# Kernel optimization log

Measured on AMD Instinct MI355X. Metric: run time of the kernel, lower is better.

## Reference

```python
import jax, jax.numpy as jnp
import numpy as np

B, C, H, W = 4, 256, 64, 64
CC = 32      # cond_channels
RATE = 2     # cond_downscale_rate
G = 8        # deformable_groups
K = 9        # 3x3 kernel positions
GN = 32      # GroupNorm groups
EPS = 1e-6


def conv2d(x, w, b, pad, groups=1):
    y = jax.lax.conv_general_dilated(x, w, (1, 1), [(pad, pad), (pad, pad)],
                                     feature_group_count=groups,
                                     dimension_numbers=('NCHW', 'OIHW', 'NCHW'))
    return y + b[None, :, None, None]


def group_norm(x, gamma, beta):
    b, c, h, w = x.shape
    xr = x.reshape(b, GN, c // GN, h, w)
    mu = xr.mean(axis=(2, 3, 4), keepdims=True)
    var = xr.var(axis=(2, 3, 4), keepdims=True)
    xn = ((xr - mu) * jax.lax.rsqrt(var + EPS)).reshape(b, c, h, w)
    return xn * gamma[None, :, None, None] + beta[None, :, None, None]


def bilinear_gather(img, y, x):
    # img [B,G,Cg,H,W]; y,x [B,G,Ho,Wo] -> [B,G,Cg,Ho,Wo], zeros outside
    Bb, Gg, Cg, Hh, Ww = img.shape
    Ho, Wo = y.shape[2], y.shape[3]
    y0 = jnp.floor(y); x0 = jnp.floor(x)
    wy1 = y - y0; wx1 = x - x0
    flat = img.reshape(Bb, Gg, Cg, Hh * Ww)

    def g(yi, xi):
        valid = (yi >= 0) & (yi <= Hh - 1) & (xi >= 0) & (xi <= Ww - 1)
        yc = jnp.clip(yi, 0, Hh - 1).astype(jnp.int32)
        xc = jnp.clip(xi, 0, Ww - 1).astype(jnp.int32)
        idx = (yc * Ww + xc).reshape(Bb, Gg, 1, Ho * Wo)
        v = jnp.take_along_axis(flat, jnp.broadcast_to(idx, (Bb, Gg, Cg, Ho * Wo)), axis=3)
        return v.reshape(Bb, Gg, Cg, Ho, Wo) * valid[:, :, None].astype(img.dtype)

    w00 = ((1 - wy1) * (1 - wx1))[:, :, None]
    w01 = ((1 - wy1) * wx1)[:, :, None]
    w10 = (wy1 * (1 - wx1))[:, :, None]
    w11 = (wy1 * wx1)[:, :, None]
    return w00 * g(y0, x0) + w01 * g(y0, x0 + 1) + w10 * g(y0 + 1, x0) + w11 * g(y0 + 1, x0 + 1)


def resize_bilinear(x, rate):
    # F.interpolate(..., mode='bilinear', align_corners=False), integer downscale
    b, c, h, w = x.shape
    ho, wo = h // rate, w // rate
    ys = (jnp.arange(ho, dtype=x.dtype) + 0.5) * rate - 0.5
    xs = (jnp.arange(wo, dtype=x.dtype) + 0.5) * rate - 0.5
    yy = jnp.broadcast_to(ys[:, None], (ho, wo))[None, None]
    xx = jnp.broadcast_to(xs[None, :], (ho, wo))[None, None]
    yy = jnp.broadcast_to(yy, (b, 1, ho, wo))
    xx = jnp.broadcast_to(xx, (b, 1, ho, wo))
    return bilinear_gather(x[:, None], yy, xx)[:, 0]


def deform_conv2d(x, offset, mask, w, b):
    # modulated deformable conv, 3x3, stride 1, pad 1 (torchvision semantics)
    Bb, Cin, Hh, Ww = x.shape
    Cg = Cin // G
    Cout = w.shape[0]
    xr = x.reshape(Bb, G, Cg, Hh, Ww)
    off = offset.reshape(Bb, G, K, 2, Hh, Ww)   # [..., (dy,dx), H, W]
    m = jax.nn.sigmoid(mask).reshape(Bb, G, K, Hh, Ww)
    base_y = jnp.arange(Hh, dtype=x.dtype)[:, None]
    base_x = jnp.arange(Ww, dtype=x.dtype)[None, :]
    acc = jnp.zeros((Bb, Cout, Hh, Ww), x.dtype)
    for k in range(K):
        kh, kw = k // 3 - 1, k % 3 - 1
        yy = base_y + kh + off[:, :, k, 0]
        xx = base_x + kw + off[:, :, k, 1]
        s = bilinear_gather(xr, yy, xx) * m[:, :, k][:, :, None]
        wk = w[:, :, kh + 1, kw + 1].reshape(Cout, G, Cg)
        acc = acc + jnp.einsum('bgchw,ogc->bohw', s, wk)
    return acc + b[None, :, None, None]


def setup_inputs() -> dict:
    key = jax.random.key(0)
    ks = jax.random.split(key, 8)
    d = {}
    d['x_main'] = jax.random.normal(ks[0], (B, C, H, W), jnp.float32)
    d['inpfeat'] = jax.random.normal(ks[1], (B, CC, H * RATE, W * RATE), jnp.float32)
    d['w1a'] = jax.random.normal(ks[2], (C, C + CC, 1, 1), jnp.float32) * (1.0 / np.sqrt(C + CC))
    d['b1a'] = jnp.zeros((C,), jnp.float32)
    d['g1'] = jnp.ones((C,), jnp.float32); d['be1'] = jnp.zeros((C,), jnp.float32)
    d['w1b'] = jax.random.normal(ks[3], (C, 1, 7, 7), jnp.float32) * (1.0 / 7.0)
    d['b1b'] = jnp.zeros((C,), jnp.float32)
    d['g2'] = jnp.ones((C,), jnp.float32); d['be2'] = jnp.zeros((C,), jnp.float32)
    d['w1c'] = jax.random.normal(ks[4], (C, C, 1, 1), jnp.float32) * (1.0 / np.sqrt(C))
    d['b1c'] = jnp.zeros((C,), jnp.float32)
    d['w2'] = jax.random.normal(ks[5], (C, C, 3, 3), jnp.float32) * (1.0 / np.sqrt(9 * C))
    d['b2'] = jnp.zeros((C,), jnp.float32)
    d['g3'] = jnp.ones((C,), jnp.float32); d['be3'] = jnp.zeros((C,), jnp.float32)
    d['w_off'] = jax.random.normal(ks[6], (3 * G * K, C, 3, 3), jnp.float32) * 0.01
    d['b_off'] = jnp.zeros((3 * G * K,), jnp.float32)
    d['w_dcn'] = jax.random.normal(ks[7], (C, C, 3, 3), jnp.float32) * (1.0 / np.sqrt(9 * C))
    d['b_dcn'] = jnp.zeros((C,), jnp.float32)
    return d


def reference(x_main, inpfeat, w1a, b1a, g1, be1, w1b, b1b, g2, be2, w1c, b1c,
              w2, b2, g3, be3, w_off, b_off, w_dcn, b_dcn):
    inp = resize_bilinear(inpfeat, RATE)                       # [B,CC,H,W]
    f = conv2d(jnp.concatenate([inp, x_main], axis=1), w1a, b1a, 0)
    f = jax.nn.silu(group_norm(f, g1, be1))
    f = conv2d(f, w1b, b1b, 3, groups=C)                       # depthwise 7x7
    f = jax.nn.silu(group_norm(f, g2, be2))
    f = conv2d(f, w1c, b1c, 0)
    off_feat = jax.nn.silu(group_norm(conv2d(f, w2, b2, 1), g3, be3))
    co = conv2d(off_feat, w_off, b_off, 1)                     # [B, 3*G*K, H, W]
    o1, o2, mk = jnp.split(co, 3, axis=1)
    offset = jnp.concatenate([o1, o2], axis=1)
    warp_feat = deform_conv2d(x_main, offset, mk, w_dcn, b_dcn)
    return warp_feat, off_feat
```

## Files before the change

kernel.cpp:

```cpp
#include <hip/hip_runtime.h>
#include <math.h>

constexpr int B = 4, C = 256, CC = 32, H = 64, W = 64, HW = H * W;
constexpr int G = 8, K = 9, GN = 32, CPG = C / GN;
constexpr int OFFC = 3 * G * K;

typedef __attribute__((ext_vector_type(8))) short short8;
typedef __attribute__((ext_vector_type(4))) float f32x4;

__device__ inline short f2bf(float f) {
  unsigned u = __builtin_bit_cast(unsigned, f);
  return (short)((u + 0x7FFFu + ((u >> 16) & 1u)) >> 16);
}
__device__ inline float bf2f(short s) {
  unsigned u = ((unsigned)(unsigned short)s) << 16;
  return __builtin_bit_cast(float, u);
}

__global__ void k_prep(const float* __restrict__ w1a, short* __restrict__ wT1a,
                       const float* __restrict__ w1c, short* __restrict__ wT1c,
                       const float* __restrict__ w2, short* __restrict__ wT2,
                       const float* __restrict__ woff, short* __restrict__ wToff,
                       const float* __restrict__ wdcn, short* __restrict__ wTd,
                       float* __restrict__ sbuf) {
  int id = blockIdx.x * 256 + threadIdx.x;
  if (id < 73728) {
    wT1a[id] = f2bf(w1a[id]);
  } else if (id < 139264) {
    int i = id - 73728;
    wT1c[i] = f2bf(w1c[i]);
  } else if (id < 204800) {
    int i = id - 139264;
    int o = i >> 8, ci = i & 255;
    #pragma unroll
    for (int k = 0; k < 9; ++k)
      wT2[((size_t)k * 256 + o) * 256 + ci] = f2bf(w2[(size_t)i * 9 + k]);
  } else if (id < 260096) {
    int i = id - 204800;
    int o = i / 256, ci = i % 256;
    #pragma unroll
    for (int k = 0; k < 9; ++k)
      wToff[((size_t)k * 216 + o) * 256 + ci] = f2bf(woff[(size_t)i * 9 + k]);
  } else if (id < 325632) {
    int i = id - 260096;
    int o = i >> 8, ci = i & 255;
    int g = ci >> 5, cg = ci & 31;
    #pragma unroll
    for (int k = 0; k < 9; ++k)
      wTd[(((size_t)g * 9 + k) * 256 + o) * 32 + cg] = f2bf(wdcn[(size_t)i * 9 + k]);
  } else if (id < 326400) {
    sbuf[id - 325632] = 0.f;
  }
}

__global__ void k_resizeT(const float* __restrict__ in, short* __restrict__ dst) {
  int t = threadIdx.x;
  int p0 = blockIdx.x * 64;
  int b = blockIdx.y;
  int px = t >> 2, cq = t & 3;
  int p = p0 + px;
  int y = p >> 6, x = p & 63;
  short8 v;
  #pragma unroll
  for (int j = 0; j < 8; ++j) {
    int c = cq * 8 + j;
    const float* src = in + ((size_t)b * CC + c) * (2 * H) * (2 * W) + (2 * y) * (2 * W) + 2 * x;
    v[j] = f2bf(0.25f * (src[0] + src[1] + src[2 * W] + src[2 * W + 1]));
  }
  *(short8*)(dst + ((size_t)b * HW + p) * 288 + cq * 8) = v;
}

__global__ void k_transpose(const float* __restrict__ src, short* __restrict__ dst,
                            int Csrc, int Cdst, int coff) {
  int t = threadIdx.x;
  int p0 = blockIdx.x * 64;
  int cc0 = blockIdx.y * 32;
  int b = blockIdx.z;
  int px = t >> 2, cq = t & 3;
  const float* s = src + ((size_t)b * Csrc + cc0 + cq * 8) * HW + p0 + px;
  short8 v;
  #pragma unroll
  for (int j = 0; j < 8; ++j) v[j] = f2bf(s[(size_t)j * HW]);
  *(short8*)(dst + ((size_t)b * HW + p0 + px) * Cdst + coff + cc0 + cq * 8) = v;
}

template<int CIN, int OUT_BF16>
__global__ __launch_bounds__(256) void k_conv1x1_mfma(
    const short* __restrict__ gT, const short* __restrict__ wT,
    const float* __restrict__ bias, void* __restrict__ outp) {
  const int tid = threadIdx.x;
  const int lane = tid & 63, wv = tid >> 6;
  const int l15 = lane & 15, l4 = lane >> 4;
  const int lin = blockIdx.x + gridDim.x * (blockIdx.y + gridDim.y * blockIdx.z);
  const int nb = gridDim.x * gridDim.y * gridDim.z;
  const int swz = (lin & 7) * (nb >> 3) + (lin >> 3);
  const int bx = swz % gridDim.x;
  const int rem = swz / gridDim.x;
  const int b = rem / gridDim.y;
  const int o0 = (rem % gridDim.y) * 64;
  const int p0 = bx * 128;

  const short* gTb = gT + (size_t)b * HW * CIN;
  const short* br[2];
  #pragma unroll
  for (int nt = 0; nt < 2; ++nt)
    br[nt] = gTb + (size_t)(p0 + wv * 32 + nt * 16 + l15) * CIN;
  const short* ar[4];
  #pragma unroll
  for (int mt = 0; mt < 4; ++mt)
    ar[mt] = wT + (size_t)(o0 + mt * 16 + l15) * CIN;

  f32x4 acc[4][2];
  #pragma unroll
  for (int mt = 0; mt < 4; ++mt)
    #pragma unroll
    for (int nt = 0; nt < 2; ++nt) acc[mt][nt] = (f32x4)0.f;

  short8 a_c[4], b_c[2], a_n[4], b_n[2];
  #pragma unroll
  for (int mt = 0; mt < 4; ++mt) a_c[mt] = *(const short8*)(ar[mt] + l4 * 8);
  #pragma unroll
  for (int nt = 0; nt < 2; ++nt) b_c[nt] = *(const short8*)(br[nt] + l4 * 8);

  for (int ck = 0; ck < CIN / 32; ++ck) {
    if (ck + 1 < CIN / 32) {
      int cin_n = (ck + 1) * 32 + l4 * 8;
      #pragma unroll
      for (int mt = 0; mt < 4; ++mt) a_n[mt] = *(const short8*)(ar[mt] + cin_n);
      #pragma unroll
      for (int nt = 0; nt < 2; ++nt) b_n[nt] = *(const short8*)(br[nt] + cin_n);
    }
    #pragma unroll
    for (int mt = 0; mt < 4; ++mt)
      #pragma unroll
      for (int nt = 0; nt < 2; ++nt)
        acc[mt][nt] = __builtin_amdgcn_mfma_f32_16x16x32_bf16(
            a_c[mt], b_c[nt], acc[mt][nt], 0, 0, 0);
    if (ck + 1 < CIN / 32) {
      #pragma unroll
      for (int mt = 0; mt < 4; ++mt) a_c[mt] = a_n[mt];
      #pragma unroll
      for (int nt = 0; nt < 2; ++nt) b_c[nt] = b_n[nt];
    }
  }

  #pragma unroll
  for (int mt = 0; mt < 4; ++mt) {
    #pragma unroll
    for (int nt = 0; nt < 2; ++nt) {
      int p = p0 + wv * 32 + nt * 16 + l15;
      if (OUT_BF16) {
        short4 vv;
        #pragma unroll
        for (int r = 0; r < 4; ++r) {
          int oo = o0 + mt * 16 + l4 * 4 + r;
          ((short*)&vv)[r] = f2bf(acc[mt][nt][r] + bias[oo]);
        }
        *(short4*)((short*)outp + ((size_t)b * HW + p) * 256 + o0 + mt * 16 + l4 * 4) = vv;
      } else {
        float* out = (float*)outp;
        #pragma unroll
        for (int r = 0; r < 4; ++r) {
          int oo = o0 + mt * 16 + l4 * 4 + r;
          out[((size_t)b * 256 + oo) * HW + p] = acc[mt][nt][r] + bias[oo];
        }
      }
    }
  }
}

template<int CIN, int COUT>
__global__ __launch_bounds__(512, 4) void k_mfma_conv9(
    const short* __restrict__ gT, const short* __restrict__ wT,
    const float* __restrict__ bias, float* __restrict__ out) {
  constexpr int POS = 4 * 66;
  constexpr int PSTR = 40;
  __shared__ short lds[2][POS * PSTR];
  const int tid = threadIdx.x;
  const int lane = tid & 63, wv = tid >> 6;
  const int l15 = lane & 15, l4 = lane >> 4;
  const int lin = blockIdx.x + gridDim.x * (blockIdx.y + gridDim.y * blockIdx.z);
  const int nb = gridDim.x * gridDim.y * gridDim.z;
  const int swz = (lin & 7) * (nb >> 3) + (lin >> 3);
  const int bx = swz % gridDim.x;
  const int rem = swz / gridDim.x;
  const int b = rem / gridDim.y;
  const int o0 = (rem % gridDim.y) * 64;
  const int p0 = bx * 128;
  const int y0 = p0 >> 6;
  const bool producer = (wv >= 4);
  const int pid = tid - 256;
  const int cwv = wv;

  const short* gTb = gT + (size_t)b * HW * CIN;

  auto stage = [&](int ck, short* sb) {
    const int ci0 = ck * 32;
    #pragma unroll
    for (int j = 0; j < 5; ++j) {
      int i = pid + j * 256;
      if (i < POS * 4) {
        int pos = i >> 2, cq = i & 3;
        short8 v = {0, 0, 0, 0, 0, 0, 0, 0};
        int r = pos / 66;
        int cx = pos - r * 66 - 1;
        int y = y0 - 1 + r;
        if ((unsigned)y < (unsigned)H && (unsigned)cx < (unsigned)W)
          v = *(const short8*)(gTb + (size_t)(y * W + cx) * CIN + ci0 + cq * 8);
        *(short8*)(sb + pos * PSTR + cq * 8) = v;
      }
    }
  };

  f32x4 acc[4][2];
  #pragma unroll
  for (int mt = 0; mt < 4; ++mt)
    #pragma unroll
    for (int nt = 0; nt < 2; ++nt) acc[mt][nt] = (f32x4)0.f;

  if (producer) stage(0, lds[0]);
  __syncthreads();
  for (int ck = 0; ck < CIN / 32; ++ck) {
    if (producer) {
      if (ck + 1 < CIN / 32) stage(ck + 1, lds[(ck + 1) & 1]);
    } else {
      const int ci0 = ck * 32;
      const short* sb = lds[ck & 1];
      for (int tap = 0; tap < 9; ++tap) {
        short8 a[4];
        #pragma unroll
        for (int mt = 0; mt < 4; ++mt) {
          int o_r = o0 + mt * 16 + l15;
          if (COUT % 64 == 0 || o_r < COUT)
            a[mt] = *(const short8*)(wT + ((size_t)tap * COUT + o_r) * CIN + ci0 + l4 * 8);
          else
            a[mt] = (short8){0, 0, 0, 0, 0, 0, 0, 0};
        }
        short8 bb[2];
        #pragma unroll
        for (int nt = 0; nt < 2; ++nt) {
          int dy = tap / 3 - 1, dx = tap % 3 - 1;
          int row = (cwv >> 1) + dy + 1;
          int col = (cwv & 1) * 32 + nt * 16 + l15 + dx + 1;
          bb[nt] = *(const short8*)(sb + (row * 66 + col) * PSTR + l4 * 8);
        }
        #pragma unroll
        for (int mt = 0; mt < 4; ++mt)
          #pragma unroll
          for (int nt = 0; nt < 2; ++nt)
            acc[mt][nt] = __builtin_amdgcn_mfma_f32_16x16x32_bf16(
                a[mt], bb[nt], acc[mt][nt], 0, 0, 0);
      }
    }
    __syncthreads();
  }

  if (!producer) {
    #pragma unroll
    for (int mt = 0; mt < 4; ++mt) {
      #pragma unroll
      for (int nt = 0; nt < 2; ++nt) {
        int p = p0 + cwv * 32 + nt * 16 + l15;
        #pragma unroll
        for (int r = 0; r < 4; ++r) {
          int oo = o0 + mt * 16 + l4 * 4 + r;
          if (COUT % 64 == 0 || oo < COUT)
            out[((size_t)b * COUT + oo) * HW + p] = acc[mt][nt][r] + bias[oo];
        }
      }
    }
  }
}

__global__ void k_gn_stats_part(const float* __restrict__ in,
                                float* __restrict__ ssum, float* __restrict__ ssq) {
  int g = blockIdx.x, b = blockIdx.y, z = blockIdx.z;
  const float4* base = (const float4*)(in + ((size_t)b * C + g * CPG) * HW) + z * 2048;
  float s = 0.f, s2 = 0.f;
  for (int i = threadIdx.x; i < 2048; i += 256) {
    float4 v = base[i];
    s  += v.x + v.y + v.z + v.w;
    s2 += v.x * v.x + v.y * v.y + v.z * v.z + v.w * v.w;
  }
  #pragma unroll
  for (int off = 32; off > 0; off >>= 1) {
    s  += __shfl_down(s, off);
    s2 += __shfl_down(s2, off);
  }
  __shared__ float sh[8];
  int wid = threadIdx.x >> 6, lane = threadIdx.x & 63;
  if (lane == 0) { sh[wid] = s; sh[4 + wid] = s2; }
  __syncthreads();
  if (threadIdx.x == 0) {
    atomicAdd(&ssum[b * GN + g], sh[0] + sh[1] + sh[2] + sh[3]);
    atomicAdd(&ssq[b * GN + g], sh[4] + sh[5] + sh[6] + sh[7]);
  }
}

template<int MODE>
__global__ void k_gnt(const float* __restrict__ in,
                      const float* __restrict__ ssum, const float* __restrict__ ssq,
                      const float* __restrict__ gamma, const float* __restrict__ beta,
                      short* __restrict__ T, float* __restrict__ outf) {
  int t = threadIdx.x;
  int p0 = blockIdx.x * 64;
  int b = blockIdx.y;
  int cc0 = blockIdx.z * 64;
  int px = t >> 2, cq = t & 3;
  int p = p0 + px;
  #pragma unroll
  for (int cc = 0; cc < 64; cc += 32) {
    int cbase = cc0 + cc + cq * 8;
    int bg = b * GN + (cbase >> 3);
    float mean = ssum[bg] * (1.f / (CPG * HW));
    float var  = ssq[bg] * (1.f / (CPG * HW)) - mean * mean;
    float inv  = rsqrtf(var + 1e-6f);
    short8 v;
    #pragma unroll
    for (int j = 0; j < 8; ++j) {
      int c = cbase + j;
      float x = in[((size_t)b * C + c) * HW + p];
      float y = (x - mean) * inv * gamma[c] + beta[c];
      y = y / (1.f + expf(-y));
      if (MODE >= 1) outf[((size_t)b * C + c) * HW + p] = y;
      v[j] = f2bf(y);
    }
    if (MODE != 2) *(short8*)(T + ((size_t)b * HW + p) * C + cbase) = v;
  }
}

__global__ void k_dw7(const float* __restrict__ in, const float* __restrict__ w,
                      const float* __restrict__ bias, float* __restrict__ out,
                      float* __restrict__ ssum, float* __restrict__ ssq) {
  int t = blockIdx.x * 256 + threadIdx.x;
  int c = blockIdx.y, b = blockIdx.z;
  int x4 = (t & 15) * 4;
  int y = t >> 4;
  const float* src = in + ((size_t)b * C + c) * HW;
  const float* wk = w + c * 49;
  float bz = bias[c];
  float a0 = bz, a1 = bz, a2 = bz, a3 = bz;
  const float4 z4 = make_float4(0.f, 0.f, 0.f, 0.f);
  #pragma unroll
  for (int ky = 0; ky < 7; ++ky) {
    int yy = y + ky - 3;
    if ((unsigned)yy >= (unsigned)H) continue;
    const float* row = src + yy * W;
    float4 A = (x4 >= 4)  ? *(const float4*)(row + x4 - 4) : z4;
    float4 Bm = *(const float4*)(row + x4);
    float4 Cx = (x4 <= 56) ? *(const float4*)(row + x4 + 4) : z4;
    float rb[12] = {A.x, A.y, A.z, A.w, Bm.x, Bm.y, Bm.z, Bm.w, Cx.x, Cx.y, Cx.z, Cx.w};
    #pragma unroll
    for (int kx = 0; kx < 7; ++kx) {
      float wv = wk[ky * 7 + kx];
      a0 += wv * rb[kx + 1];
      a1 += wv * rb[kx + 2];
      a2 += wv * rb[kx + 3];
      a3 += wv * rb[kx + 4];
    }
  }
  *(float4*)(out + ((size_t)b * C + c) * HW + y * W + x4) = make_float4(a0, a1, a2, a3);
  float s = a0 + a1 + a2 + a3;
  float s2 = a0 * a0 + a1 * a1 + a2 * a2 + a3 * a3;
  #pragma unroll
  for (int off = 32; off > 0; off >>= 1) {
    s  += __shfl_down(s, off);
    s2 += __shfl_down(s2, off);
  }
  __shared__ float sh[8];
  int wid = threadIdx.x >> 6, lane = threadIdx.x & 63;
  if (lane == 0) { sh[wid] = s; sh[4 + wid] = s2; }
  __syncthreads();
  if (threadIdx.x == 0) {
    atomicAdd(&ssum[b * GN + (c >> 3)], sh[0] + sh[1] + sh[2] + sh[3]);
    atomicAdd(&ssq[b * GN + (c >> 3)], sh[4] + sh[5] + sh[6] + sh[7]);
  }
}

__global__ __launch_bounds__(512, 4) void k_deform_mfma(
    const short* __restrict__ xmT, const float* __restrict__ co,
    const short* __restrict__ wT, const float* __restrict__ bias,
    float* __restrict__ out) {
  constexpr int PSTR = 40;
  __shared__ short s[2][K * 32 * PSTR];
  const int tid = threadIdx.x;
  const int lane = tid & 63, wv = tid >> 6;
  const int l15 = lane & 15, l4 = lane >> 4;
  const int lin = blockIdx.x + gridDim.x * blockIdx.y;
  const int nb = gridDim.x * gridDim.y;
  const int swz = (lin & 7) * (nb >> 3) + (lin >> 3);
  const int b = swz / (HW / 32);
  const int p0 = (swz % (HW / 32)) * 32;
  const bool producer = (wv >= 4);
  const int o0 = wv * 64;
  const int pid = tid - 256;

  const short* xb = xmT + (size_t)b * HW * C;
  const float* cob = co + (size_t)b * OFFC * HW;

  float cdy[5], cdx[5], cml[5];

  auto loadco = [&](int g) {
    #pragma unroll
    for (int j = 0; j < 5; ++j) {
      if (j == 4 && pid >= 128) continue;
      int i = pid + j * 256;
      int tap = i >> 7, pl = (i & 127) >> 2;
      int p = p0 + pl;
      cdy[j] = cob[(size_t)((g * K + tap) * 2) * HW + p];
      cdx[j] = cob[(size_t)((g * K + tap) * 2 + 1) * HW + p];
      cml[j] = cob[(size_t)(144 + g * K + tap) * HW + p];
    }
  };

  auto stage = [&](int g, short* sb) {
    #pragma unroll
    for (int j = 0; j < 5; ++j) {
      if (j == 4 && pid >= 128) continue;
      int i = pid + j * 256;
      int tap = i >> 7, r = i & 127, pl = r >> 2, cq = r & 3;
      int p = p0 + pl;
      float m = 1.f / (1.f + expf(-cml[j]));
      int kh = tap / 3 - 1, kw = tap % 3 - 1;
      int py = p >> 6, px = p & 63;
      float yy = (float)(py + kh) + cdy[j];
      float xx = (float)(px + kw) + cdx[j];
      float yf = floorf(yy), xf = floorf(xx);
      float wy = yy - yf, wx = xx - xf;
      int y0 = (int)yf, x0 = (int)xf;
      bool yv0 = (unsigned)y0 < (unsigned)H, yv1 = (unsigned)(y0 + 1) < (unsigned)H;
      bool xv0 = (unsigned)x0 < (unsigned)W, xv1 = (unsigned)(x0 + 1) < (unsigned)W;
      int yc0 = min(max(y0, 0), H - 1), yc1 = min(max(y0 + 1, 0), H - 1);
      int xc0 = min(max(x0, 0), W - 1), xc1 = min(max(x0 + 1, 0), W - 1);
      float w00 = (yv0 && xv0) ? (1.f - wy) * (1.f - wx) * m : 0.f;
      float w01 = (yv0 && xv1) ? (1.f - wy) * wx * m : 0.f;
      float w10 = (yv1 && xv0) ? wy * (1.f - wx) * m : 0.f;
      float w11 = (yv1 && xv1) ? wy * wx * m : 0.f;
      const short* xg = xb + g * 32 + cq * 8;
      short8 v00 = *(const short8*)(xg + (size_t)(yc0 * W + xc0) * C);
      short8 v01 = *(const short8*)(xg + (size_t)(yc0 * W + xc1) * C);
      short8 v10 = *(const short8*)(xg + (size_t)(yc1 * W + xc0) * C);
      short8 v11 = *(const short8*)(xg + (size_t)(yc1 * W + xc1) * C);
      short8 rr;
      #pragma unroll
      for (int jj = 0; jj < 8; ++jj)
        rr[jj] = f2bf(w00 * bf2f(v00[jj]) + w01 * bf2f(v01[jj]) +
                      w10 * bf2f(v10[jj]) + w11 * bf2f(v11[jj]));
      *(short8*)(sb + (tap * 32 + pl) * PSTR + cq * 8) = rr;
    }
  };

  f32x4 acc[4][2];
  #pragma unroll
  for (int mt = 0; mt < 4; ++mt)
    #pragma unroll
    for (int nt = 0; nt < 2; ++nt) acc[mt][nt] = (f32x4)0.f;

  if (producer) {
    loadco(0);
    stage(0, s[0]);
    loadco(1);
  }
  __syncthreads();
  for (int g = 0; g < G; ++g) {
    if (producer) {
      if (g < G - 1) {
        stage(g + 1, s[(g + 1) & 1]);
        if (g < G - 2) loadco(g + 2);
      }
    } else {
      const short* sb = s[g & 1];
      const short* wg = wT + (size_t)g * K * 256 * 32;
      short8 a_c[4], a_n[4];
      #pragma unroll
      for (int mt = 0; mt < 4; ++mt)
        a_c[mt] = *(const short8*)(wg + (size_t)(o0 + mt * 16 + l15) * 32 + l4 * 8);
      for (int k = 0; k < K; ++k) {
        short8 bb0 = *(const short8*)(sb + (k * 32 + l15) * PSTR + l4 * 8);
        short8 bb1 = *(const short8*)(sb + (k * 32 + 16 + l15) * PSTR + l4 * 8);
        if (k < K - 1) {
          #pragma unroll
          for (int mt = 0; mt < 4; ++mt)
            a_n[mt] = *(const short8*)(wg + (size_t)((k + 1) * 256 + o0 + mt * 16 + l15) * 32 + l4 * 8);
        }
        #pragma unroll
        for (int mt = 0; mt < 4; ++mt) {
          acc[mt][0] = __builtin_amdgcn_mfma_f32_16x16x32_bf16(a_c[mt], bb0, acc[mt][0], 0, 0, 0);
          acc[mt][1] = __builtin_amdgcn_mfma_f32_16x16x32_bf16(a_c[mt], bb1, acc[mt][1], 0, 0, 0);
        }
        if (k < K - 1) {
          #pragma unroll
          for (int mt = 0; mt < 4; ++mt) a_c[mt] = a_n[mt];
        }
      }
    }
    __syncthreads();
  }

  if (!producer) {
    #pragma unroll
    for (int mt = 0; mt < 4; ++mt) {
      #pragma unroll
      for (int nt = 0; nt < 2; ++nt) {
        int p = p0 + nt * 16 + l15;
        #pragma unroll
        for (int r = 0; r < 4; ++r) {
          int oo = o0 + mt * 16 + l4 * 4 + r;
          out[((size_t)b * C + oo) * HW + p] = acc[mt][nt][r] + bias[oo];
        }
      }
    }
  }
}

extern "C" void kernel_launch(void* const* d_in, const int* in_sizes, int n_in,
                              void* d_out, int out_size, void* d_ws, size_t ws_size,
                              hipStream_t stream) {
  const float* x_main  = (const float*)d_in[0];
  const float* inpfeat = (const float*)d_in[1];
  const float* w1a = (const float*)d_in[2];
  const float* b1a = (const float*)d_in[3];
  const float* g1  = (const float*)d_in[4];
  const float* be1 = (const float*)d_in[5];
  const float* w1b = (const float*)d_in[6];
  const float* b1b = (const float*)d_in[7];
  const float* g2  = (const float*)d_in[8];
  const float* be2 = (const float*)d_in[9];
  const float* w1c = (const float*)d_in[10];
  const float* b1c = (const float*)d_in[11];
  const float* w2  = (const float*)d_in[12];
  const float* b2  = (const float*)d_in[13];
  const float* g3  = (const float*)d_in[14];
  const float* be3 = (const float*)d_in[15];
  const float* w_off = (const float*)d_in[16];
  const float* b_off = (const float*)d_in[17];
  const float* w_dcn = (const float*)d_in[18];
  const float* b_dcn = (const float*)d_in[19];

  float* warp_out = (float*)d_out;
  float* off_out  = warp_out + (size_t)B * C * HW;

  char* ws = (char*)d_ws;
  float* r_inp = (float*)ws;
  float* fA    = (float*)(ws + (2u << 20));
  short* T288  = (short*)(ws + (2u << 20) + (16u << 20));
  char*  wbase = ws + (2u << 20) + (16u << 20) + 9437184;
  short* wT1a  = (short*)(wbase);
  short* wT1c  = (short*)(wbase + 147456);
  short* wT2   = (short*)(wbase + 147456 + 131072);
  short* wToff = (short*)(wbase + 147456 + 131072 + 1179648);
  float* sbuf  = (float*)(wbase + 147456 + 131072 + 1179648 + 995328);
  float* ssum1 = sbuf,       *ssq1 = sbuf + 128;
  float* ssum2 = sbuf + 256, *ssq2 = sbuf + 384;
  float* ssum3 = sbuf + 512, *ssq3 = sbuf + 640;
  short* wTd   = (short*)r_inp;
  short* Tc    = (short*)fA;
  short* T2    = T288;
  float* fB = warp_out;
  float* co = fA;

  k_prep<<<dim3(1275), 256, 0, stream>>>(w1a, wT1a, w1c, wT1c, w2, wT2,
                                         w_off, wToff, w_dcn, wTd, sbuf);
  k_resizeT<<<dim3(HW / 64, B), 256, 0, stream>>>(inpfeat, T288);
  k_transpose<<<dim3(HW / 64, 8, B), 256, 0, stream>>>(x_main, T288, C, 288, 32);
  k_conv1x1_mfma<288, 0><<<dim3(HW / 128, 4, B), 256, 0, stream>>>(T288, wT1a, b1a, fA);
  k_gn_stats_part<<<dim3(GN, B, 4), 256, 0, stream>>>(fA, ssum1, ssq1);
  k_gnt<2><<<dim3(HW / 64, B, 4), 256, 0, stream>>>(fA, ssum1, ssq1, g1, be1, nullptr, fA);
  k_dw7<<<dim3(HW / 1024, C, B), 256, 0, stream>>>(fA, w1b, b1b, fB, ssum2, ssq2);
  k_gnt<0><<<dim3(HW / 64, B, 4), 256, 0, stream>>>(fB, ssum2, ssq2, g2, be2, T2, nullptr);
  k_conv1x1_mfma<256, 1><<<dim3(HW / 128, 4, B), 256, 0, stream>>>(T2, wT1c, b1c, Tc);
  k_mfma_conv9<256, 256><<<dim3(HW / 128, 4, B), 512, 0, stream>>>(Tc, wT2, b2, fB);
  k_gn_stats_part<<<dim3(GN, B, 4), 256, 0, stream>>>(fB, ssum3, ssq3);
  k_gnt<1><<<dim3(HW / 64, B, 4), 256, 0, stream>>>(fB, ssum3, ssq3, g3, be3, T2, off_out);
  k_mfma_conv9<256, 216><<<dim3(HW / 128, 4, B), 512, 0, stream>>>(T2, wToff, b_off, co);
  k_transpose<<<dim3(HW / 64, 8, B), 256, 0, stream>>>(x_main, T288, C, 256, 0);
  k_deform_mfma<<<dim3(HW / 32, B), 512, 0, stream>>>(T288, co, wTd, b_dcn, warp_out);
}
```

Measured before the change: 347.6 us.

## Stage conv3x3 weights through LDS with finer-grained producer/consumer pipeline

The 3x3 MFMA convolution kernel now has its producer waves copy weight tiles into a double-buffered LDS region, in chunks of three taps per 32-channel slice. Consumer waves no longer read weights directly from global memory. The input-tile staging is split across the three tap-row sub-steps so producer work is spread evenly over more, smaller pipeline stages. The goal is to take global-memory weight latency off the MFMA path, at the cost of more LDS (about 55 KB per block), which may limit occupancy, and three times as many block barriers.

```diff
diff --git a/kernel.cpp b/kernel.cpp
--- a/kernel.cpp
+++ b/kernel.cpp
@@ -175,7 +175,10 @@
     const float* __restrict__ bias, float* __restrict__ out) {
   constexpr int POS = 4 * 66;
   constexpr int PSTR = 40;
-  __shared__ short lds[2][POS * PSTR];
+  constexpr int WSTR = 36;
+  constexpr int NCC = 3 * (CIN / 32);
+  __shared__ short ib[2][POS * PSTR];
+  __shared__ short wb[2][192 * WSTR];
   const int tid = threadIdx.x;
   const int lane = tid & 63, wv = tid >> 6;
   const int l15 = lane & 15, l4 = lane >> 4;
@@ -194,12 +197,13 @@
 
   const short* gTb = gT + (size_t)b * HW * CIN;
 
-  auto stage = [&](int ck, short* sb) {
+  auto stageI = [&](int ck, int c, short* sb) {
     const int ci0 = ck * 32;
     #pragma unroll
-    for (int j = 0; j < 5; ++j) {
-      int i = pid + j * 256;
-      if (i < POS * 4) {
+    for (int j = 0; j < 2; ++j) {
+      int q = pid + j * 256;
+      if (q < 352) {
+        int i = c * 352 + q;
         int pos = i >> 2, cq = i & 3;
         short8 v = {0, 0, 0, 0, 0, 0, 0, 0};
         int r = pos / 66;
@@ -211,6 +215,20 @@
       }
     }
   };
+  auto stageW = [&](int cc, short* sb) {
+    const int ck = cc / 3, c = cc % 3;
+    const int ci0 = ck * 32;
+    #pragma unroll
+    for (int j = 0; j < 3; ++j) {
+      int i = pid + j * 256;
+      int row = i >> 2, cq = i & 3;
+      int tl = row >> 6, oo = o0 + (row & 63);
+      short8 v = {0, 0, 0, 0, 0, 0, 0, 0};
+      if (COUT % 64 == 0 || oo < COUT)
+        v = *(const short8*)(wT + ((size_t)(3 * c + tl) * COUT + oo) * CIN + ci0 + cq * 8);
+      *(short8*)(sb + row * WSTR + cq * 8) = v;
+    }
+  };
 
   f32x4 acc[4][2];
   #pragma unroll
@@ -218,31 +236,35 @@
     #pragma unroll
     for (int nt = 0; nt < 2; ++nt) acc[mt][nt] = (f32x4)0.f;
 
-  if (producer) stage(0, lds[0]);
+  if (producer) {
+    stageI(0, 0, ib[0]);
+    stageI(0, 1, ib[0]);
+    stageI(0, 2, ib[0]);
+    stageW(0, wb[0]);
+  }
   __syncthreads();
-  for (int ck = 0; ck < CIN / 32; ++ck) {
+  for (int cc = 0; cc < NCC; ++cc) {
+    const int ck = cc / 3, c = cc % 3;
     if (producer) {
-      if (ck + 1 < CIN / 32) stage(ck + 1, lds[(ck + 1) & 1]);
+      if (cc + 1 < NCC) stageW(cc + 1, wb[(cc + 1) & 1]);
+      if (ck + 1 < CIN / 32) stageI(ck + 1, c, ib[(ck + 1) & 1]);
     } else {
-      const int ci0 = ck * 32;
-      const short* sb = lds[ck & 1];
-      for (int tap = 0; tap < 9; ++tap) {
+      const short* sbw = wb[cc & 1];
+      const short* sbi = ib[ck & 1];
+      #pragma unroll
+      for (int tl = 0; tl < 3; ++tl) {
+        const int tap = 3 * c + tl;
         short8 a[4];
         #pragma unroll
-        for (int mt = 0; mt < 4; ++mt) {
-          int o_r = o0 + mt * 16 + l15;
-          if (COUT % 64 == 0 || o_r < COUT)
-            a[mt] = *(const short8*)(wT + ((size_t)tap * COUT + o_r) * CIN + ci0 + l4 * 8);
-          else
-            a[mt] = (short8){0, 0, 0, 0, 0, 0, 0, 0};
-        }
+        for (int mt = 0; mt < 4; ++mt)
+          a[mt] = *(const short8*)(sbw + (tl * 64 + mt * 16 + l15) * WSTR + l4 * 8);
         short8 bb[2];
         #pragma unroll
         for (int nt = 0; nt < 2; ++nt) {
           int dy = tap / 3 - 1, dx = tap % 3 - 1;
           int row = (cwv >> 1) + dy + 1;
           int col = (cwv & 1) * 32 + nt * 16 + l15 + dx + 1;
-          bb[nt] = *(const short8*)(sb + (row * 66 + col) * PSTR + l4 * 8);
+          bb[nt] = *(const short8*)(sbi + (row * 66 + col) * PSTR + l4 * 8);
         }
         #pragma unroll
         for (int mt = 0; mt < 4; ++mt)
```

New measurement: 385.6 us. +10.9%, slower.
